# Optimization experiments

Hardware: AMD Instinct MI355X
Metric: run time of the kernel (lower is better)

The kernel has to match this reference:

```python
import jax, jax.numpy as jnp
import numpy as np

STRIDE = 1  # conv stride from __init__


def setup_inputs() -> dict:
    key = jax.random.key(0)
    k1, k2, k3 = jax.random.split(key, 3)
    prot1 = jax.random.normal(k1, (4, 1024, 8, 64), dtype=jnp.float32)
    prot2 = jax.random.normal(k2, (4, 1024, 8, 64), dtype=jnp.float32)
    # W: (no_filters, no_channels, no_dims, window_size)
    W = jax.random.normal(k3, (32, 8, 64, 7), dtype=jnp.float32)
    return {"prot1": prot1, "prot2": prot2, "W": W}


def _project(x, W, stride):
    """Fused equivalent of unfold + broadcast-mul + sum over (C, window).

    x: (N, H, C, D), W: (F, C, D, w) -> (N, F, H', D) with H' = (H - w)//stride + 1.
    This is a grouped 1D conv: D groups, each mixing C input channels into F outputs.
    """
    N, H, C, D = x.shape
    Fn, _, _, w = W.shape
    xg = jnp.transpose(x, (0, 3, 2, 1)).reshape(N, D * C, H)        # (N, D*C, H)
    Wg = jnp.transpose(W, (2, 0, 1, 3)).reshape(D * Fn, C, w)       # (D*F, C, w)
    out = jax.lax.conv_general_dilated(
        xg, Wg, window_strides=(stride,), padding='VALID',
        dimension_numbers=('NCH', 'OIH', 'NCH'), feature_group_count=D)
    Hp = out.shape[-1]
    return jnp.transpose(out.reshape(N, D, Fn, Hp), (0, 2, 3, 1))   # (N, F, H', D)


def reference(prot1, prot2, W):
    q1 = _project(prot1, W, STRIDE)   # (N, F, H1', D)
    q2 = _project(prot2, W, STRIDE)   # (N, F, H2', D)
    H1p, H2p = q1.shape[2], q2.shape[2]
    scale = jnp.sqrt(jnp.asarray(H1p * H2p, dtype=q1.dtype))
    att = jnp.einsum('nfhd,nfgd->nfhg', q1, q2) / scale             # (N, F, H1', H2')
    a = jax.nn.softmax(att, axis=3)
    p1 = jnp.einsum('nfhg,nfgd->nfhd', a, q2)                       # (N, F, H1', D)
    # NB: source does transpose(att, 2, 2) (a no-op) and multiplies the SAME
    # softmax matrix by the UPDATED p1folds; we reproduce that faithfully.
    p2 = jnp.einsum('nfhg,nfgd->nfhd', a, p1)                       # (N, F, H1', D)
    out1 = jnp.tanh(jnp.transpose(p1, (0, 2, 1, 3)))                # (N, H1', F, D)
    out2 = jnp.tanh(jnp.transpose(p2, (0, 2, 1, 3)))
    # Dropout is identity in eval mode (and dropout_p=0.0 here).
    return (out1, out2)
```

## Files before the change

### kernel.cpp

```cpp
#include <hip/hip_runtime.h>
#include <math.h>

typedef __bf16 bf16_t;
typedef bf16_t bf16x4 __attribute__((ext_vector_type(4)));
typedef bf16_t bf16x8 __attribute__((ext_vector_type(8)));
typedef float  f32x16 __attribute__((ext_vector_type(16)));

#define HH 1024
#define CC 8
#define DD 64
#define FF 32
#define WW 7
#define HP 1018
#define HPAD 1024
#define NF 128
#define QOUT (NF*HP*DD)
#define QWS ((size_t)NF*HPAD*DD)
#define LSTR 72

#if __has_builtin(__builtin_amdgcn_exp2f)
#define EXP2(x) __builtin_amdgcn_exp2f(x)
#else
#define EXP2(x) __expf((x) * 0.6931471805599453f)
#endif

__global__ __launch_bounds__(256) void wprep_kernel(
    const float* __restrict__ Wt, float* __restrict__ Wp)
{
    const int idx = blockIdx.x * 256 + threadIdx.x;
    if (idx < FF*CC*DD*WW) {
        const int j = idx % WW;
        int t = idx / WW;
        const int d = t % DD; t /= DD;
        const int c = t % CC;
        const int f = t / CC;
        Wp[((f*CC + c)*WW + j)*DD + d] = Wt[idx];
    }
}

__global__ __launch_bounds__(256) void conv_kernel(
    const float* __restrict__ x1, const float* __restrict__ x2,
    const float* __restrict__ Wp, bf16_t* __restrict__ q1, bf16_t* __restrict__ q2)
{
    __shared__ float xs[38*512];
    const float* x = blockIdx.z ? x2 : x1;
    bf16_t* q = blockIdx.z ? q2 : q1;
    const int n = blockIdx.y;
    const int hb = blockIdx.x * 32;
    const int tid = threadIdx.x;

    const float4* xg = (const float4*)(x + (size_t)n*HH*512);
    for (int i = tid; i < 38*128; i += 256) {
        const int row = hb + (i >> 7);
        float4 v = {0.f, 0.f, 0.f, 0.f};
        if (row < HH) v = xg[(size_t)row*128 + (i & 127)];
        *(float4*)&xs[(size_t)i*4] = v;
    }
    __syncthreads();

    const int d = tid & 63;
    const int fq = tid >> 6;
    for (int fi = 0; fi < 8; ++fi) {
        const int f = fq*8 + fi;
        float w[CC][WW];
#pragma unroll
        for (int c = 0; c < CC; ++c)
#pragma unroll
            for (int j = 0; j < WW; ++j)
                w[c][j] = Wp[((f*CC + c)*WW + j)*DD + d];
#pragma unroll
        for (int hc = 0; hc < 2; ++hc) {
            float acc[16];
#pragma unroll
            for (int i = 0; i < 16; ++i) acc[i] = 0.f;
#pragma unroll
            for (int rr = 0; rr < 22; ++rr) {
                float xv[CC];
#pragma unroll
                for (int c = 0; c < CC; ++c)
                    xv[c] = xs[(hc*16 + rr)*512 + c*64 + d];
#pragma unroll
                for (int j = 0; j < WW; ++j) {
                    const int i = rr - j;
                    if (i >= 0 && i < 16) {
#pragma unroll
                        for (int c = 0; c < CC; ++c)
                            acc[i] = fmaf(xv[c], w[c][j], acc[i]);
                    }
                }
            }
#pragma unroll
            for (int i = 0; i < 16; ++i) {
                const int h = hb + hc*16 + i;
                const float v = (h < HP) ? acc[i] : 0.f;
                q[((size_t)(n*FF + f)*HPAD + h)*DD + d] = (bf16_t)v;
            }
        }
    }
}

__device__ __forceinline__ float fast_tanh(float x) {
    const float t = __expf(2.f * x);
    return (t - 1.f) / (t + 1.f);
}

template<int MODE>
__global__ __launch_bounds__(256, 2) void flash(
    const bf16_t* __restrict__ q1, const bf16_t* __restrict__ q2,
    const bf16_t* __restrict__ vsrc, bf16_t* __restrict__ p1out,
    float* __restrict__ out)
{
    __shared__ __align__(16) bf16_t As[64*LSTR];
    __shared__ __align__(16) bf16_t Vt[64*LSTR];

    const int head = blockIdx.y;
    const int n = head >> 5, f = head & 31;
    const int tid = threadIdx.x;
    const int w = tid >> 6;
    const int lane = tid & 63;
    const int lid = lane & 31;
    const int half = lane >> 5;
    const int hb = blockIdx.x * 256 + w * 64;

    const size_t qoff = (size_t)head * HPAD * DD;
    const float SC = 1.442695041f / 1018.f;

    const int gq = tid >> 4;
    const int dq = tid & 15;
    const int cgb = 4*((gq>>1)&1) + 8*(gq&1) + 16*(gq>>2);

    bf16x8 bq1[2][4];
#pragma unroll
    for (int nt = 0; nt < 2; ++nt)
#pragma unroll
        for (int kt = 0; kt < 4; ++kt)
            bq1[nt][kt] = *(const bf16x8*)&q1[qoff + (size_t)(hb + 32*nt + lid)*DD + 16*kt + 8*half];

    f32x16 O[2][2] = {};
    float lacc[2] = {0.f, 0.f};

    bf16x4 rA[4], rV[4];
#pragma unroll
    for (int i = 0; i < 4; ++i) {
        rA[i] = *(const bf16x4*)&q2[qoff + (size_t)(4*gq + i)*DD + 4*dq];
        if (MODE == 1)
            rV[i] = *(const bf16x4*)&vsrc[qoff + (size_t)(4*gq + i)*DD + 4*dq];
    }

    for (int g0 = 0; g0 < HPAD; g0 += 64) {
        __syncthreads();
#pragma unroll
        for (int i = 0; i < 4; ++i)
            *(bf16x4*)&As[(4*gq + i)*LSTR + 4*dq] = rA[i];
        {
            const bf16x4* rv = (MODE == 1) ? rV : rA;
#pragma unroll
            for (int j = 0; j < 4; ++j) {
                bf16x4 c = { rv[0][j], rv[1][j], rv[2][j], rv[3][j] };
                *(bf16x4*)&Vt[(4*dq + j)*LSTR + cgb] = c;
            }
        }
        __syncthreads();

        if (g0 + 64 < HPAD) {
            const int gn = g0 + 64;
#pragma unroll
            for (int i = 0; i < 4; ++i) {
                rA[i] = *(const bf16x4*)&q2[qoff + (size_t)(gn + 4*gq + i)*DD + 4*dq];
                if (MODE == 1)
                    rV[i] = *(const bf16x4*)&vsrc[qoff + (size_t)(gn + 4*gq + i)*DD + 4*dq];
            }
        }

        const bool tail = (g0 + 64 > HP);

#pragma unroll
        for (int mt = 0; mt < 2; ++mt) {
            f32x16 C[2] = {};
#pragma unroll
            for (int kt = 0; kt < 4; ++kt) {
                bf16x8 a = *(const bf16x8*)&As[(32*mt + lid)*LSTR + 16*kt + 8*half];
                C[0] = __builtin_amdgcn_mfma_f32_32x32x16_bf16(a, bq1[0][kt], C[0], 0,0,0);
                C[1] = __builtin_amdgcn_mfma_f32_32x32x16_bf16(a, bq1[1][kt], C[1], 0,0,0);
            }
            bf16x8 af[2][2];
#pragma unroll
            for (int nt = 0; nt < 2; ++nt) {
                float ls = 0.f;
#pragma unroll
                for (int s = 0; s < 16; ++s) {
                    float e = EXP2(C[nt][s] * SC);
                    if (tail) {
                        const int gg = g0 + 32*mt + (s&3) + 8*(s>>2) + 4*half;
                        if (gg >= HP) e = 0.f;
                    }
                    ls += e;
                    af[nt][s>>3][s&7] = (bf16_t)e;
                }
                lacc[nt] += ls;
            }
#pragma unroll
            for (int u = 0; u < 2; ++u) {
#pragma unroll
                for (int dt = 0; dt < 2; ++dt) {
                    bf16x8 b = *(const bf16x8*)&Vt[(32*dt + lid)*LSTR + 32*mt + 16*u + 8*half];
                    O[0][dt] = __builtin_amdgcn_mfma_f32_32x32x16_bf16(af[0][u], b, O[0][dt], 0,0,0);
                    O[1][dt] = __builtin_amdgcn_mfma_f32_32x32x16_bf16(af[1][u], b, O[1][dt], 0,0,0);
                }
            }
        }
    }

    float linv[2];
#pragma unroll
    for (int nt = 0; nt < 2; ++nt) {
        const float l = lacc[nt] + __shfl_xor(lacc[nt], 32);
        linv[nt] = 1.f / l;
    }
#pragma unroll
    for (int ht = 0; ht < 2; ++ht) {
#pragma unroll
        for (int s = 0; s < 16; ++s) {
            const int R = (s&3) + 8*(s>>2) + 4*half;
            const float li = __shfl(linv[ht], R);
            const int hg = hb + 32*ht + R;
            if (hg < HP) {
#pragma unroll
                for (int dt = 0; dt < 2; ++dt) {
                    const int d = 32*dt + lid;
                    const float val = O[ht][dt][s] * li;
                    out[(((size_t)n*HP + hg)*FF + f)*DD + d] = fast_tanh(val);
                    if (MODE == 0)
                        p1out[qoff + (size_t)hg*DD + d] = (bf16_t)val;
                }
            }
        }
    }
}

extern "C" void kernel_launch(void* const* d_in, const int* in_sizes, int n_in,
                              void* d_out, int out_size, void* d_ws, size_t ws_size,
                              hipStream_t stream)
{
    const float* prot1 = (const float*)d_in[0];
    const float* prot2 = (const float*)d_in[1];
    const float* Wt    = (const float*)d_in[2];
    float* out = (float*)d_out;

    bf16_t* q1b = (bf16_t*)d_ws;
    bf16_t* q2b = q1b + QWS;
    bf16_t* p1b = q2b + QWS;
    float* Wp   = (float*)(p1b + QWS);

    wprep_kernel<<<dim3(448), 256, 0, stream>>>(Wt, Wp);
    conv_kernel<<<dim3(32, 4, 2), 256, 0, stream>>>(prot1, prot2, Wp, q1b, q2b);
    flash<0><<<dim3(4, NF), 256, 0, stream>>>(q1b, q2b, q2b, p1b, out);
    flash<1><<<dim3(4, NF), 256, 0, stream>>>(q1b, q2b, p1b, p1b, out + QOUT);
}
```

Measured before the change: 224.5 us.

## Halve rows per wave in flash kernels, double grid, swizzle V tile in LDS

Each wave of the attention kernels now handles 32 query rows instead of 64, so the grid doubles to 8x128 blocks and launch bounds allow 4 blocks per CU. The transposed V tile in shared memory changes from a padded row stride to an XOR-swizzled layout to avoid bank conflicts. The aim is more resident waves and better occupancy for a small workload (512 blocks). In exchange, each K/V tile is loaded and transposed into LDS twice as many times overall, and there is less MFMA work per LDS read.

```diff
diff --git a/kernel.cpp b/kernel.cpp
--- a/kernel.cpp
+++ b/kernel.cpp
@@ -24,6 +24,10 @@
 #define EXP2(x) __expf((x) * 0.6931471805599453f)
 #endif
 
+__device__ __forceinline__ int vaddr(int row, int col) {
+    return row*64 + ((((col>>3) ^ (row&7) ^ ((row>>2)&7)))<<3) + (col&7);
+}
+
 __global__ __launch_bounds__(256) void wprep_kernel(
     const float* __restrict__ Wt, float* __restrict__ Wp)
 {
@@ -105,13 +109,13 @@
 }
 
 template<int MODE>
-__global__ __launch_bounds__(256, 2) void flash(
+__global__ __launch_bounds__(256, 4) void flash(
     const bf16_t* __restrict__ q1, const bf16_t* __restrict__ q2,
     const bf16_t* __restrict__ vsrc, bf16_t* __restrict__ p1out,
     float* __restrict__ out)
 {
     __shared__ __align__(16) bf16_t As[64*LSTR];
-    __shared__ __align__(16) bf16_t Vt[64*LSTR];
+    __shared__ __align__(16) bf16_t Vt[64*64];
 
     const int head = blockIdx.y;
     const int n = head >> 5, f = head & 31;
@@ -120,24 +124,23 @@
     const int lane = tid & 63;
     const int lid = lane & 31;
     const int half = lane >> 5;
-    const int hb = blockIdx.x * 256 + w * 64;
+    const int hb = blockIdx.x * 128 + w * 32;
 
     const size_t qoff = (size_t)head * HPAD * DD;
     const float SC = 1.442695041f / 1018.f;
+    const int vswz = (lid & 7) ^ (lid >> 2);
 
     const int gq = tid >> 4;
     const int dq = tid & 15;
     const int cgb = 4*((gq>>1)&1) + 8*(gq&1) + 16*(gq>>2);
 
-    bf16x8 bq1[2][4];
-#pragma unroll
-    for (int nt = 0; nt < 2; ++nt)
-#pragma unroll
-        for (int kt = 0; kt < 4; ++kt)
-            bq1[nt][kt] = *(const bf16x8*)&q1[qoff + (size_t)(hb + 32*nt + lid)*DD + 16*kt + 8*half];
-
-    f32x16 O[2][2] = {};
-    float lacc[2] = {0.f, 0.f};
+    bf16x8 bq1[4];
+#pragma unroll
+    for (int kt = 0; kt < 4; ++kt)
+        bq1[kt] = *(const bf16x8*)&q1[qoff + (size_t)(hb + lid)*DD + 16*kt + 8*half];
+
+    f32x16 O[2] = {};
+    float lacc = 0.f;
 
     bf16x4 rA[4], rV[4];
 #pragma unroll
@@ -157,7 +160,7 @@
 #pragma unroll
             for (int j = 0; j < 4; ++j) {
                 bf16x4 c = { rv[0][j], rv[1][j], rv[2][j], rv[3][j] };
-                *(bf16x4*)&Vt[(4*dq + j)*LSTR + cgb] = c;
+                *(bf16x4*)&Vt[vaddr(4*dq + j, cgb)] = c;
             }
         }
         __syncthreads();
@@ -176,63 +179,52 @@
 
 #pragma unroll
         for (int mt = 0; mt < 2; ++mt) {
-            f32x16 C[2] = {};
+            f32x16 C = {};
 #pragma unroll
             for (int kt = 0; kt < 4; ++kt) {
                 bf16x8 a = *(const bf16x8*)&As[(32*mt + lid)*LSTR + 16*kt + 8*half];
-                C[0] = __builtin_amdgcn_mfma_f32_32x32x16_bf16(a, bq1[0][kt], C[0], 0,0,0);
-                C[1] = __builtin_amdgcn_mfma_f32_32x32x16_bf16(a, bq1[1][kt], C[1], 0,0,0);
-            }
-            bf16x8 af[2][2];
-#pragma unroll
-            for (int nt = 0; nt < 2; ++nt) {
-                float ls = 0.f;
-#pragma unroll
-                for (int s = 0; s < 16; ++s) {
-                    float e = EXP2(C[nt][s] * SC);
-                    if (tail) {
-                        const int gg = g0 + 32*mt + (s&3) + 8*(s>>2) + 4*half;
-                        if (gg >= HP) e = 0.f;
-                    }
-                    ls += e;
-                    af[nt][s>>3][s&7] = (bf16_t)e;
+                C = __builtin_amdgcn_mfma_f32_32x32x16_bf16(a, bq1[kt], C, 0,0,0);
+            }
+            bf16x8 af[2];
+            float ls = 0.f;
+#pragma unroll
+            for (int s = 0; s < 16; ++s) {
+                float e = EXP2(C[s] * SC);
+                if (tail) {
+                    const int gg = g0 + 32*mt + (s&3) + 8*(s>>2) + 4*half;
+                    if (gg >= HP) e = 0.f;
                 }
-                lacc[nt] += ls;
-            }
+                ls += e;
+                af[s>>3][s&7] = (bf16_t)e;
+            }
+            lacc += ls;
 #pragma unroll
             for (int u = 0; u < 2; ++u) {
 #pragma unroll
                 for (int dt = 0; dt < 2; ++dt) {
-                    bf16x8 b = *(const bf16x8*)&Vt[(32*dt + lid)*LSTR + 32*mt + 16*u + 8*half];
-                    O[0][dt] = __builtin_amdgcn_mfma_f32_32x32x16_bf16(af[0][u], b, O[0][dt], 0,0,0);
-                    O[1][dt] = __builtin_amdgcn_mfma_f32_32x32x16_bf16(af[1][u], b, O[1][dt], 0,0,0);
+                    const int chunk = (4*mt + 2*u + half) ^ vswz;
+                    bf16x8 b = *(const bf16x8*)&Vt[(32*dt + lid)*64 + chunk*8];
+                    O[dt] = __builtin_amdgcn_mfma_f32_32x32x16_bf16(af[u], b, O[dt], 0,0,0);
                 }
             }
         }
     }
 
-    float linv[2];
-#pragma unroll
-    for (int nt = 0; nt < 2; ++nt) {
-        const float l = lacc[nt] + __shfl_xor(lacc[nt], 32);
-        linv[nt] = 1.f / l;
-    }
-#pragma unroll
-    for (int ht = 0; ht < 2; ++ht) {
-#pragma unroll
-        for (int s = 0; s < 16; ++s) {
-            const int R = (s&3) + 8*(s>>2) + 4*half;
-            const float li = __shfl(linv[ht], R);
-            const int hg = hb + 32*ht + R;
-            if (hg < HP) {
-#pragma unroll
-                for (int dt = 0; dt < 2; ++dt) {
-                    const int d = 32*dt + lid;
-                    const float val = O[ht][dt][s] * li;
-                    out[(((size_t)n*HP + hg)*FF + f)*DD + d] = fast_tanh(val);
-                    if (MODE == 0)
-                        p1out[qoff + (size_t)hg*DD + d] = (bf16_t)val;
-                }
+    const float l = lacc + __shfl_xor(lacc, 32);
+    const float linv = 1.f / l;
+#pragma unroll
+    for (int s = 0; s < 16; ++s) {
+        const int R = (s&3) + 8*(s>>2) + 4*half;
+        const float li = __shfl(linv, R);
+        const int hg = hb + R;
+        if (hg < HP) {
+#pragma unroll
+            for (int dt = 0; dt < 2; ++dt) {
+                const int d = 32*dt + lid;
+                const float val = O[dt][s] * li;
+                out[(((size_t)n*HP + hg)*FF + f)*DD + d] = fast_tanh(val);
+                if (MODE == 0)
+                    p1out[qoff + (size_t)hg*DD + d] = (bf16_t)val;
             }
         }
     }
@@ -254,6 +246,6 @@
 
     wprep_kernel<<<dim3(448), 256, 0, stream>>>(Wt, Wp);
     conv_kernel<<<dim3(32, 4, 2), 256, 0, stream>>>(prot1, prot2, Wp, q1b, q2b);
-    flash<0><<<dim3(4, NF), 256, 0, stream>>>(q1b, q2b, q2b, p1b, out);
-    flash<1><<<dim3(4, NF), 256, 0, stream>>>(q1b, q2b, p1b, p1b, out + QOUT);
-}
+    flash<0><<<dim3(8, NF), 256, 0, stream>>>(q1b, q2b, q2b, p1b, out);
+    flash<1><<<dim3(8, NF), 256, 0, stream>>>(q1b, q2b, p1b, p1b, out + QOUT);
+}
```

Result: slower. 240.0 us (+6.9%).

## Load K operand directly from global, swizzle V tile, transpose conv smem layout

Applied to the files above, without the earlier changes.

The flash kernel now loads the q2 K-operand fragments straight from global memory into registers, prefetching the next tile, instead of staging them through a padded LDS buffer. The transposed V tile uses an XOR-swizzled 64-wide layout in place of the padded stride to avoid bank conflicts. The conv kernel stores x in smem channel-innermost so each thread reads its 8 channels with two float4 loads, at the cost of scalar scattered smem writes. The p1 output now writes zeros for the padded rows, keeping MODE 1 correct, at the cost of more VGPR pressure from the prefetched fragments.

```diff
diff --git a/kernel.cpp b/kernel.cpp
--- a/kernel.cpp
+++ b/kernel.cpp
@@ -16,13 +16,16 @@
 #define NF 128
 #define QOUT (NF*HP*DD)
 #define QWS ((size_t)NF*HPAD*DD)
-#define LSTR 72
 
 #if __has_builtin(__builtin_amdgcn_exp2f)
 #define EXP2(x) __builtin_amdgcn_exp2f(x)
 #else
 #define EXP2(x) __expf((x) * 0.6931471805599453f)
 #endif
+
+__device__ __forceinline__ int vaddr(int row, int col) {
+    return row*64 + ((((col>>3) ^ (row&7) ^ ((row>>2)&7)))<<3) + (col&7);
+}
 
 __global__ __launch_bounds__(256) void wprep_kernel(
     const float* __restrict__ Wt, float* __restrict__ Wp)
@@ -54,7 +57,13 @@
         const int row = hb + (i >> 7);
         float4 v = {0.f, 0.f, 0.f, 0.f};
         if (row < HH) v = xg[(size_t)row*128 + (i & 127)];
-        *(float4*)&xs[(size_t)i*4] = v;
+        const int r = i >> 7;
+        const int c = (i & 127) >> 4;
+        const int d0 = ((i & 127) & 15) * 4;
+        xs[r*512 + (d0+0)*8 + c] = v.x;
+        xs[r*512 + (d0+1)*8 + c] = v.y;
+        xs[r*512 + (d0+2)*8 + c] = v.z;
+        xs[r*512 + (d0+3)*8 + c] = v.w;
     }
     __syncthreads();
 
@@ -75,10 +84,9 @@
             for (int i = 0; i < 16; ++i) acc[i] = 0.f;
 #pragma unroll
             for (int rr = 0; rr < 22; ++rr) {
-                float xv[CC];
-#pragma unroll
-                for (int c = 0; c < CC; ++c)
-                    xv[c] = xs[(hc*16 + rr)*512 + c*64 + d];
+                const float4 a = *(const float4*)&xs[(hc*16 + rr)*512 + d*8 + 0];
+                const float4 b = *(const float4*)&xs[(hc*16 + rr)*512 + d*8 + 4];
+                const float xv[8] = {a.x, a.y, a.z, a.w, b.x, b.y, b.z, b.w};
 #pragma unroll
                 for (int j = 0; j < WW; ++j) {
                     const int i = rr - j;
@@ -110,8 +118,7 @@
     const bf16_t* __restrict__ vsrc, bf16_t* __restrict__ p1out,
     float* __restrict__ out)
 {
-    __shared__ __align__(16) bf16_t As[64*LSTR];
-    __shared__ __align__(16) bf16_t Vt[64*LSTR];
+    __shared__ __align__(16) bf16_t Vt[64*64];
 
     const int head = blockIdx.y;
     const int n = head >> 5, f = head & 31;
@@ -124,11 +131,14 @@
 
     const size_t qoff = (size_t)head * HPAD * DD;
     const float SC = 1.442695041f / 1018.f;
+    const int vswz = (lid & 7) ^ (lid >> 2);
 
     const int gq = tid >> 4;
     const int dq = tid & 15;
     const int cgb = 4*((gq>>1)&1) + 8*(gq&1) + 16*(gq>>2);
 
+    const bf16_t* vptr = (MODE == 1) ? vsrc : q2;
+
     bf16x8 bq1[2][4];
 #pragma unroll
     for (int nt = 0; nt < 2; ++nt)
@@ -136,40 +146,34 @@
         for (int kt = 0; kt < 4; ++kt)
             bq1[nt][kt] = *(const bf16x8*)&q1[qoff + (size_t)(hb + 32*nt + lid)*DD + 16*kt + 8*half];
 
+    bf16x8 aq[2][4];
+#pragma unroll
+    for (int mt = 0; mt < 2; ++mt)
+#pragma unroll
+        for (int kt = 0; kt < 4; ++kt)
+            aq[mt][kt] = *(const bf16x8*)&q2[qoff + (size_t)(32*mt + lid)*DD + 16*kt + 8*half];
+
+    bf16x4 rV[4];
+#pragma unroll
+    for (int i = 0; i < 4; ++i)
+        rV[i] = *(const bf16x4*)&vptr[qoff + (size_t)(4*gq + i)*DD + 4*dq];
+
     f32x16 O[2][2] = {};
     float lacc[2] = {0.f, 0.f};
 
-    bf16x4 rA[4], rV[4];
-#pragma unroll
-    for (int i = 0; i < 4; ++i) {
-        rA[i] = *(const bf16x4*)&q2[qoff + (size_t)(4*gq + i)*DD + 4*dq];
-        if (MODE == 1)
-            rV[i] = *(const bf16x4*)&vsrc[qoff + (size_t)(4*gq + i)*DD + 4*dq];
-    }
-
     for (int g0 = 0; g0 < HPAD; g0 += 64) {
         __syncthreads();
 #pragma unroll
-        for (int i = 0; i < 4; ++i)
-            *(bf16x4*)&As[(4*gq + i)*LSTR + 4*dq] = rA[i];
-        {
-            const bf16x4* rv = (MODE == 1) ? rV : rA;
-#pragma unroll
-            for (int j = 0; j < 4; ++j) {
-                bf16x4 c = { rv[0][j], rv[1][j], rv[2][j], rv[3][j] };
-                *(bf16x4*)&Vt[(4*dq + j)*LSTR + cgb] = c;
-            }
+        for (int j = 0; j < 4; ++j) {
+            bf16x4 c = { rV[0][j], rV[1][j], rV[2][j], rV[3][j] };
+            *(bf16x4*)&Vt[vaddr(4*dq + j, cgb)] = c;
         }
         __syncthreads();
 
         if (g0 + 64 < HPAD) {
-            const int gn = g0 + 64;
-#pragma unroll
-            for (int i = 0; i < 4; ++i) {
-                rA[i] = *(const bf16x4*)&q2[qoff + (size_t)(gn + 4*gq + i)*DD + 4*dq];
-                if (MODE == 1)
-                    rV[i] = *(const bf16x4*)&vsrc[qoff + (size_t)(gn + 4*gq + i)*DD + 4*dq];
-            }
+#pragma unroll
+            for (int i = 0; i < 4; ++i)
+                rV[i] = *(const bf16x4*)&vptr[qoff + (size_t)(g0 + 64 + 4*gq + i)*DD + 4*dq];
         }
 
         const bool tail = (g0 + 64 > HP);
@@ -179,9 +183,13 @@
             f32x16 C[2] = {};
 #pragma unroll
             for (int kt = 0; kt < 4; ++kt) {
-                bf16x8 a = *(const bf16x8*)&As[(32*mt + lid)*LSTR + 16*kt + 8*half];
-                C[0] = __builtin_amdgcn_mfma_f32_32x32x16_bf16(a, bq1[0][kt], C[0], 0,0,0);
-                C[1] = __builtin_amdgcn_mfma_f32_32x32x16_bf16(a, bq1[1][kt], C[1], 0,0,0);
+                C[0] = __builtin_amdgcn_mfma_f32_32x32x16_bf16(aq[mt][kt], bq1[0][kt], C[0], 0,0,0);
+                C[1] = __builtin_amdgcn_mfma_f32_32x32x16_bf16(aq[mt][kt], bq1[1][kt], C[1], 0,0,0);
+            }
+            if (g0 + 64 < HPAD) {
+#pragma unroll
+                for (int kt = 0; kt < 4; ++kt)
+                    aq[mt][kt] = *(const bf16x8*)&q2[qoff + (size_t)(g0 + 64 + 32*mt + lid)*DD + 16*kt + 8*half];
             }
             bf16x8 af[2][2];
 #pragma unroll
@@ -203,7 +211,8 @@
             for (int u = 0; u < 2; ++u) {
 #pragma unroll
                 for (int dt = 0; dt < 2; ++dt) {
-                    bf16x8 b = *(const bf16x8*)&Vt[(32*dt + lid)*LSTR + 32*mt + 16*u + 8*half];
+                    const int chunk = (4*mt + 2*u + half) ^ vswz;
+                    bf16x8 b = *(const bf16x8*)&Vt[(32*dt + lid)*64 + chunk*8];
                     O[0][dt] = __builtin_amdgcn_mfma_f32_32x32x16_bf16(af[0][u], b, O[0][dt], 0,0,0);
                     O[1][dt] = __builtin_amdgcn_mfma_f32_32x32x16_bf16(af[1][u], b, O[1][dt], 0,0,0);
                 }
@@ -224,15 +233,14 @@
             const int R = (s&3) + 8*(s>>2) + 4*half;
             const float li = __shfl(linv[ht], R);
             const int hg = hb + 32*ht + R;
-            if (hg < HP) {
-#pragma unroll
-                for (int dt = 0; dt < 2; ++dt) {
-                    const int d = 32*dt + lid;
-                    const float val = O[ht][dt][s] * li;
+#pragma unroll
+            for (int dt = 0; dt < 2; ++dt) {
+                const int d = 32*dt + lid;
+                const float val = O[ht][dt][s] * li;
+                if (hg < HP)
                     out[(((size_t)n*HP + hg)*FF + f)*DD + d] = fast_tanh(val);
-                    if (MODE == 0)
-                        p1out[qoff + (size_t)hg*DD + d] = (bf16_t)val;
-                }
+                if (MODE == 0)
+                    p1out[qoff + (size_t)hg*DD + d] = (bf16_t)(hg < HP ? val : 0.f);
             }
         }
     }
```

Result: no change. 220.6 us (-1.8%).
